# Kernel tuning notes

Measured on AMD Instinct MI355X. Metric: run time of the kernel, lower is better.

The kernel has to match this reference:

```python
import jax, jax.numpy as jnp
import numpy as np

EPS = 1e-09  # from module __init__ eps


def setup_inputs() -> dict:
    key = jax.random.key(0)
    k1, k2 = jax.random.split(key)
    N = 384 * 384
    input1 = jax.random.normal(k1, (1, 32, 384, 384), dtype=jnp.float32)
    input2 = jax.random.randint(k2, (N, 48), 0, N, dtype=jnp.int64)
    return {"input1": input1, "input2": input2}


def reference(input1, input2):
    # input1: [*, a, b, c] -> UU: [N, a] with N = b*c (pixels), a = features
    a, b, c = input1.shape[1], input1.shape[2], input1.shape[3]
    UU = input1.reshape(a, b * c).T  # [N, a]
    J = input2.shape[0]
    nbr = UU[input2]                      # [J, K, a] gather of neighbor features
    diff = UU[:J][:, None, :] - nbr       # [J, K, a]
    msd = jnp.mean(diff * diff, axis=-1)  # [J, K] mean squared distance
    D = -jnp.sqrt(msd + EPS)              # [J, K]
    W = jax.nn.softmax(D, axis=1)         # softmax over K neighbors
    return W
```

## Files before the change

### kernel.cpp

```cpp
#include <hip/hip_runtime.h>
#include <hip/hip_fp16.h>


#define EPS 1e-9f

__global__ __launch_bounds__(256) void transpose_half_kernel(
    const float* __restrict__ in, __half* __restrict__ UU, int N) {
  const int p = blockIdx.x * 256 + threadIdx.x;
  if (p >= N) return;
  __half h[32];
#pragma unroll
  for (int f = 0; f < 32; ++f) h[f] = __float2half_rn(in[(size_t)f * N + p]);
  uint4* dst = (uint4*)(UU + (size_t)p * 32);
#pragma unroll
  for (int r = 0; r < 4; ++r) {
    __half2 a = __halves2half2(h[8 * r + 0], h[8 * r + 1]);
    __half2 b = __halves2half2(h[8 * r + 2], h[8 * r + 3]);
    __half2 c = __halves2half2(h[8 * r + 4], h[8 * r + 5]);
    __half2 d = __halves2half2(h[8 * r + 6], h[8 * r + 7]);
    dst[r] = make_uint4(*(unsigned*)&a, *(unsigned*)&b, *(unsigned*)&c, *(unsigned*)&d);
  }
}

__device__ __forceinline__ void acc8(const uint4& b, const float* aj, int base,
                                     float& s) {
  float2 f0 = __half22float2(*(const __half2*)&b.x);
  float2 f1 = __half22float2(*(const __half2*)&b.y);
  float2 f2 = __half22float2(*(const __half2*)&b.z);
  float2 f3 = __half22float2(*(const __half2*)&b.w);
  float d;
  d = aj[base + 0] - f0.x; s += d * d;
  d = aj[base + 1] - f0.y; s += d * d;
  d = aj[base + 2] - f1.x; s += d * d;
  d = aj[base + 3] - f1.y; s += d * d;
  d = aj[base + 4] - f2.x; s += d * d;
  d = aj[base + 5] - f2.y; s += d * d;
  d = aj[base + 6] - f3.x; s += d * d;
  d = aj[base + 7] - f3.y; s += d * d;
}

__global__ __launch_bounds__(256) void dist_softmax_kernel(
    const __half* __restrict__ UU, const int* __restrict__ idx,
    float* __restrict__ out, int J) {
  const int wave = blockIdx.x * 4 + (threadIdx.x >> 6);
  const int lane = threadIdx.x & 63;
  if (wave >= J) return;

  const uint4* uj = (const uint4*)(UU + (size_t)wave * 32);
  float aj[32];
#pragma unroll
  for (int r = 0; r < 4; ++r) {
    uint4 v = uj[r];
    float2 f0 = __half22float2(*(const __half2*)&v.x);
    float2 f1 = __half22float2(*(const __half2*)&v.y);
    float2 f2 = __half22float2(*(const __half2*)&v.z);
    float2 f3 = __half22float2(*(const __half2*)&v.w);
    aj[8 * r + 0] = f0.x; aj[8 * r + 1] = f0.y;
    aj[8 * r + 2] = f1.x; aj[8 * r + 3] = f1.y;
    aj[8 * r + 4] = f2.x; aj[8 * r + 5] = f2.y;
    aj[8 * r + 6] = f3.x; aj[8 * r + 7] = f3.y;
  }

  float D = -INFINITY;
  if (lane < 48) {
    const int nb = idx[(size_t)wave * 48 + lane];
    const uint4* un = (const uint4*)(UU + (size_t)nb * 32);
    uint4 b0 = un[0], b1 = un[1], b2 = un[2], b3 = un[3];
    float s = 0.f;
    acc8(b0, aj, 0, s);
    acc8(b1, aj, 8, s);
    acc8(b2, aj, 16, s);
    acc8(b3, aj, 24, s);
    D = -sqrtf(s * (1.0f / 32.0f) + EPS);
  }

  float m = D;
#pragma unroll
  for (int off = 32; off; off >>= 1) m = fmaxf(m, __shfl_xor(m, off));
  float e = (lane < 48) ? __expf(D - m) : 0.f;
  float ssum = e;
#pragma unroll
  for (int off = 32; off; off >>= 1) ssum += __shfl_xor(ssum, off);
  if (lane < 48) out[(size_t)wave * 48 + lane] = e / ssum;
}

extern "C" void kernel_launch(void* const* d_in, const int* in_sizes, int n_in,
                              void* d_out, int out_size, void* d_ws, size_t ws_size,
                              hipStream_t stream) {
  const float* in1 = (const float*)d_in[0];
  const int* idx = (const int*)d_in[1];
  float* out = (float*)d_out;
  __half* UU = (__half*)d_ws;

  const int N = in_sizes[0] / 32;
  const int J = in_sizes[1] / 48;

  transpose_half_kernel<<<(N + 255) / 256, 256, 0, stream>>>(in1, UU, N);

  dist_softmax_kernel<<<(J + 3) / 4, 256, 0, stream>>>(UU, idx, out, J);
}
```

Baseline: 166.7 us.

## Pack four rows per wave with 16-lane groups and fp16 dot2 distance

Restructures the distance-softmax kernel so each 64-lane wave serves four rows. Each 16-lane group handles one row and three neighbors per lane, which removes the 16 idle lanes per wave and shortens the shuffle reductions to 16 lanes. The squared distance now subtracts in packed fp16 and accumulates with the fdot2 builtin instead of converting every element to fp32. The fp16 subtraction lowers precision somewhat, and each lane now issues three gathers, which raises register pressure.

```diff
diff --git a/kernel.cpp b/kernel.cpp
--- a/kernel.cpp
+++ b/kernel.cpp
@@ -4,8 +4,11 @@
 
 #define EPS 1e-9f
 
+typedef _Float16 h2 __attribute__((ext_vector_type(2)));
+union V16 { uint4 u; h2 h[4]; };
+
 __global__ __launch_bounds__(256) void transpose_half_kernel(
-    const float* __restrict__ in, __half* __restrict__ UU, int N) {
+    const float* __restrict__ in, _Float16* __restrict__ UU, int N) {
   const int p = blockIdx.x * 256 + threadIdx.x;
   if (p >= N) return;
   __half h[32];
@@ -22,66 +25,80 @@
   }
 }
 
-__device__ __forceinline__ void acc8(const uint4& b, const float* aj, int base,
-                                     float& s) {
-  float2 f0 = __half22float2(*(const __half2*)&b.x);
-  float2 f1 = __half22float2(*(const __half2*)&b.y);
-  float2 f2 = __half22float2(*(const __half2*)&b.z);
-  float2 f3 = __half22float2(*(const __half2*)&b.w);
-  float d;
-  d = aj[base + 0] - f0.x; s += d * d;
-  d = aj[base + 1] - f0.y; s += d * d;
-  d = aj[base + 2] - f1.x; s += d * d;
-  d = aj[base + 3] - f1.y; s += d * d;
-  d = aj[base + 4] - f2.x; s += d * d;
-  d = aj[base + 5] - f2.y; s += d * d;
-  d = aj[base + 6] - f3.x; s += d * d;
-  d = aj[base + 7] - f3.y; s += d * d;
+__device__ __forceinline__ float dot2acc(h2 d, float s) {
+#if __has_builtin(__builtin_amdgcn_fdot2)
+  return __builtin_amdgcn_fdot2(d, d, s, false);
+#else
+  float x = (float)d.x, y = (float)d.y;
+  return s + x * x + y * y;
+#endif
 }
 
 __global__ __launch_bounds__(256) void dist_softmax_kernel(
-    const __half* __restrict__ UU, const int* __restrict__ idx,
+    const _Float16* __restrict__ UU, const int* __restrict__ idx,
     float* __restrict__ out, int J) {
-  const int wave = blockIdx.x * 4 + (threadIdx.x >> 6);
-  const int lane = threadIdx.x & 63;
-  if (wave >= J) return;
+  const int tid = threadIdx.x;
+  const int wave = blockIdx.x * 4 + (tid >> 6);
+  const int lane = tid & 63;
+  const int g = lane >> 4;
+  const int sub = lane & 15;
+  const int j = wave * 4 + g;
+  if (j >= J) return;
 
-  const uint4* uj = (const uint4*)(UU + (size_t)wave * 32);
-  float aj[32];
+  const int* ij = idx + (size_t)j * 48;
+  const int n0 = ij[sub];
+  const int n1 = ij[sub + 16];
+  const int n2 = ij[sub + 32];
+
+  const V16* uj = (const V16*)(UU + (size_t)j * 32);
+  const V16* q0 = (const V16*)(UU + (size_t)n0 * 32);
+  const V16* q1 = (const V16*)(UU + (size_t)n1 * 32);
+  const V16* q2 = (const V16*)(UU + (size_t)n2 * 32);
+
+  V16 a[4], b0[4], b1[4], b2[4];
+#pragma unroll
+  for (int r = 0; r < 4; ++r) a[r].u = uj[r].u;
+#pragma unroll
+  for (int r = 0; r < 4; ++r) b0[r].u = q0[r].u;
+#pragma unroll
+  for (int r = 0; r < 4; ++r) b1[r].u = q1[r].u;
+#pragma unroll
+  for (int r = 0; r < 4; ++r) b2[r].u = q2[r].u;
+
+  float s0 = 0.f, s1 = 0.f, s2 = 0.f;
 #pragma unroll
   for (int r = 0; r < 4; ++r) {
-    uint4 v = uj[r];
-    float2 f0 = __half22float2(*(const __half2*)&v.x);
-    float2 f1 = __half22float2(*(const __half2*)&v.y);
-    float2 f2 = __half22float2(*(const __half2*)&v.z);
-    float2 f3 = __half22float2(*(const __half2*)&v.w);
-    aj[8 * r + 0] = f0.x; aj[8 * r + 1] = f0.y;
-    aj[8 * r + 2] = f1.x; aj[8 * r + 3] = f1.y;
-    aj[8 * r + 4] = f2.x; aj[8 * r + 5] = f2.y;
-    aj[8 * r + 6] = f3.x; aj[8 * r + 7] = f3.y;
+#pragma unroll
+    for (int i = 0; i < 4; ++i) {
+      const h2 av = a[r].h[i];
+      h2 d0 = av - b0[r].h[i];
+      h2 d1 = av - b1[r].h[i];
+      h2 d2 = av - b2[r].h[i];
+      s0 = dot2acc(d0, s0);
+      s1 = dot2acc(d1, s1);
+      s2 = dot2acc(d2, s2);
+    }
   }
 
-  float D = -INFINITY;
-  if (lane < 48) {
-    const int nb = idx[(size_t)wave * 48 + lane];
-    const uint4* un = (const uint4*)(UU + (size_t)nb * 32);
-    uint4 b0 = un[0], b1 = un[1], b2 = un[2], b3 = un[3];
-    float s = 0.f;
-    acc8(b0, aj, 0, s);
-    acc8(b1, aj, 8, s);
-    acc8(b2, aj, 16, s);
-    acc8(b3, aj, 24, s);
-    D = -sqrtf(s * (1.0f / 32.0f) + EPS);
-  }
+  float D0 = -sqrtf(s0 * (1.0f / 32.0f) + EPS);
+  float D1 = -sqrtf(s1 * (1.0f / 32.0f) + EPS);
+  float D2 = -sqrtf(s2 * (1.0f / 32.0f) + EPS);
 
-  float m = D;
+  float m = fmaxf(D0, fmaxf(D1, D2));
 #pragma unroll
-  for (int off = 32; off; off >>= 1) m = fmaxf(m, __shfl_xor(m, off));
-  float e = (lane < 48) ? __expf(D - m) : 0.f;
-  float ssum = e;
+  for (int off = 8; off; off >>= 1) m = fmaxf(m, __shfl_xor(m, off));
+  float e0 = __expf(D0 - m);
+  float e1 = __expf(D1 - m);
+  float e2 = __expf(D2 - m);
+  float t = e0 + e1 + e2;
 #pragma unroll
-  for (int off = 32; off; off >>= 1) ssum += __shfl_xor(ssum, off);
-  if (lane < 48) out[(size_t)wave * 48 + lane] = e / ssum;
+  for (int off = 8; off; off >>= 1) t += __shfl_xor(t, off);
+  const float inv = 1.0f / t;
+
+  float* oj = out + (size_t)j * 48;
+  oj[sub] = e0 * inv;
+  oj[sub + 16] = e1 * inv;
+  oj[sub + 32] = e2 * inv;
 }
 
 extern "C" void kernel_launch(void* const* d_in, const int* in_sizes, int n_in,
@@ -90,12 +107,12 @@
   const float* in1 = (const float*)d_in[0];
   const int* idx = (const int*)d_in[1];
   float* out = (float*)d_out;
-  __half* UU = (__half*)d_ws;
+  _Float16* UU = (_Float16*)d_ws;
 
   const int N = in_sizes[0] / 32;
   const int J = in_sizes[1] / 48;
 
   transpose_half_kernel<<<(N + 255) / 256, 256, 0, stream>>>(in1, UU, N);
 
-  dist_softmax_kernel<<<(J + 3) / 4, 256, 0, stream>>>(UU, idx, out, J);
+  dist_softmax_kernel<<<(J + 15) / 16, 256, 0, stream>>>(UU, idx, out, J);
 }
```

Result: slower. 207.5 us (+24.4%).
